# Kernel optimization log

Hardware: AMD Instinct MI355X
Metric: run time of the kernel (lower is better)

The kernel has to match this reference:

```python
import jax, jax.numpy as jnp
import numpy as np

H = 128; W = 128          # BEV grid (row_num_embed = col_num_embed = 128)
B = 1
CIN = 384; D = 256; NH = 8; NP = 4; NF = 128  # NF = num_feats of pos encoding
NLAYERS = 4               # 3 cross + 1 self


def setup_inputs() -> dict:
    key = jax.random.key(0)
    ks = jax.random.split(key, 32)
    s = 0.02
    rn = lambda k, shp: (jax.random.normal(k, shp, dtype=jnp.float32) * s)
    z = lambda shp: jnp.zeros(shp, jnp.float32)
    inp = {
        'query': jax.random.normal(ks[0], (B, CIN, H, W), jnp.float32),
        'value': jax.random.normal(ks[1], (B, CIN, H, W), jnp.float32),
        # 1x1 conv input projections (out, in)
        'conv_q_w': rn(ks[2], (D, CIN)), 'conv_q_b': z((D,)),
        'conv_v_w': rn(ks[3], (D, CIN)), 'conv_v_b': z((D,)),
        # learned positional embedding tables
        'row_embed': rn(ks[4], (H, NF)), 'col_embed': rn(ks[5], (W, NF)),
        # pre-attention linear layers (in, out)
        'lin_q_w': rn(ks[6], (D, D)), 'lin_q_b': z((D,)),
        'lin_v_w': rn(ks[7], (D, D)), 'lin_v_b': z((D,)),
        # stacked MSDeformAttn params for 4 layers
        'msda_off_w': rn(ks[8], (NLAYERS, D, NH * NP * 2)), 'msda_off_b': z((NLAYERS, NH * NP * 2)),
        'msda_aw_w': rn(ks[9], (NLAYERS, D, NH * NP)), 'msda_aw_b': z((NLAYERS, NH * NP)),
        'msda_vp_w': rn(ks[10], (NLAYERS, D, D)), 'msda_vp_b': z((NLAYERS, D)),
        'msda_op_w': rn(ks[11], (NLAYERS, D, D)), 'msda_op_b': z((NLAYERS, D)),
        # output MLP: 256 -> 128 -> 64 -> 384 with LayerNorm+ReLU between
        'out_w1': rn(ks[12], (D, D // 2)), 'out_b1': z((D // 2,)),
        'ln1_g': jnp.ones((D // 2,), jnp.float32), 'ln1_b': z((D // 2,)),
        'out_w2': rn(ks[13], (D // 2, D // 4)), 'out_b2': z((D // 4,)),
        'ln2_g': jnp.ones((D // 4,), jnp.float32), 'ln2_b': z((D // 4,)),
        'out_w3': rn(ks[14], (D // 4, CIN)), 'out_b3': z((CIN,)),
    }
    return inp


def _ln(x, g, b):
    mu = jnp.mean(x, -1, keepdims=True)
    var = jnp.mean(jnp.square(x - mu), -1, keepdims=True)
    return (x - mu) * jax.lax.rsqrt(var + 1e-5) * g + b


def reference(query, value, conv_q_w, conv_q_b, conv_v_w, conv_v_b, row_embed, col_embed,
              lin_q_w, lin_q_b, lin_v_w, lin_v_b,
              msda_off_w, msda_off_b, msda_aw_w, msda_aw_b,
              msda_vp_w, msda_vp_b, msda_op_w, msda_op_b,
              out_w1, out_b1, ln1_g, ln1_b, out_w2, out_b2, ln2_g, ln2_b, out_w3, out_b3):
    Bv, Cin, Hh, Ww = query.shape
    Nq = Hh * Ww
    HD = D // NH
    # 1x1 convs = per-pixel channel matmul; layout (Nq, B, D) = flatten(2).permute(2,0,1)
    q = jnp.einsum('bchw,dc->hwbd', query, conv_q_w).reshape(Nq, Bv, D) + conv_q_b
    v = jnp.einsum('bchw,dc->hwbd', value, conv_v_w).reshape(Nq, Bv, D) + conv_v_b
    # LearnedPositionalEncoding: cat([col_embed(x), row_embed(y)], -1)
    pos = jnp.concatenate([
        jnp.broadcast_to(col_embed[None, :Ww], (Hh, Ww, NF)),
        jnp.broadcast_to(row_embed[:Hh, None], (Hh, Ww, NF))], -1).reshape(Nq, 1, D)
    q = q @ lin_q_w + lin_q_b
    v = v @ lin_v_w + lin_v_b
    # reference points (pixel centers, normalized, (x, y) order)
    ry = (jnp.arange(Hh, dtype=q.dtype) + 0.5) / Hh
    rx = (jnp.arange(Ww, dtype=q.dtype) + 0.5) / Ww
    gx, gy = jnp.meshgrid(rx, ry, indexing='xy')  # (H, W)
    ref = jnp.stack([gx, gy], -1).reshape(1, Nq, 2)
    inv_wh = jnp.array([1.0 / Ww, 1.0 / Hh], dtype=q.dtype)

    def msda_layer(q_in, v_in, i):
        qp = q_in + pos                                   # query + query_pos
        val = (v_in @ msda_vp_w[i] + msda_vp_b[i]).transpose(1, 0, 2).reshape(Bv, Hh, Ww, NH, HD)
        off = (qp @ msda_off_w[i] + msda_off_b[i]).transpose(1, 0, 2).reshape(Bv, Nq, NH, NP, 2)
        aw = jax.nn.softmax((qp @ msda_aw_w[i] + msda_aw_b[i]).transpose(1, 0, 2)
                            .reshape(Bv, Nq, NH, NP), axis=-1)
        loc = ref[:, :, None, None, :] + off * inv_wh     # (B, Nq, NH, NP, 2) in [0,1]
        # bilinear sampling, zero padding, align_corners=False (grid_sample semantics)
        x = loc[..., 0] * Ww - 0.5
        y = loc[..., 1] * Hh - 0.5
        x0f = jnp.floor(x); y0f = jnp.floor(y)
        lx = (x - x0f).transpose(0, 2, 1, 3)              # (B, NH, Nq, NP)
        ly = (y - y0f).transpose(0, 2, 1, 3)
        x0 = x0f.astype(jnp.int32).transpose(0, 2, 1, 3)
        y0 = y0f.astype(jnp.int32).transpose(0, 2, 1, 3)
        vflat = val.transpose(0, 3, 1, 2, 4).reshape(Bv, NH, Hh * Ww, HD)
        awt = aw.transpose(0, 2, 1, 3)                    # (B, NH, Nq, NP)

        def corner(yi, xi, w):
            valid = (yi >= 0) & (yi < Hh) & (xi >= 0) & (xi < Ww)
            idx = (jnp.clip(yi, 0, Hh - 1) * Ww + jnp.clip(xi, 0, Ww - 1)).reshape(Bv, NH, Nq * NP, 1)
            g = jnp.take_along_axis(vflat, idx, axis=2).reshape(Bv, NH, Nq, NP, HD)
            return g * (w * valid.astype(w.dtype) * awt)[..., None]

        out = (corner(y0, x0, (1 - lx) * (1 - ly))
               + corner(y0, x0 + 1, lx * (1 - ly))
               + corner(y0 + 1, x0, (1 - lx) * ly)
               + corner(y0 + 1, x0 + 1, lx * ly)).sum(3)  # (B, NH, Nq, HD)
        out = out.transpose(2, 0, 1, 3).reshape(Nq, Bv, D)
        return out @ msda_op_w[i] + msda_op_b[i] + q_in   # residual (dropout=identity, eval)

    for i in range(3):                                    # cross layers: value features
        q = msda_layer(q, v, i)
    q = msda_layer(q, q, 3)                               # self layer: value = query

    h1 = jax.nn.relu(_ln(q @ out_w1 + out_b1, ln1_g, ln1_b))
    h2 = jax.nn.relu(_ln(h1 @ out_w2 + out_b2, ln2_g, ln2_b))
    out = h2 @ out_w3 + out_b3                            # (Nq, B, Cin)
    return out.transpose(1, 2, 0).reshape(Bv, Cin, Hh, Ww)
```

## Files before the change

kernel.cpp:

```cpp
#include <hip/hip_runtime.h>
#include <hip/hip_bf16.h>

#define NQ   16384
#define DIM  256

using bf16 = __hip_bfloat16;
using bf16x8 = __attribute__((ext_vector_type(8))) short;
using f32x4  = __attribute__((ext_vector_type(4))) float;

__device__ __forceinline__ float b2f(bf16 x) { return __bfloat162float(x); }
__device__ __forceinline__ bf16  f2b(float x) { return __float2bfloat16(x); }
__device__ __forceinline__ unsigned short f2bb(float x) {
    bf16 h = __float2bfloat16(x);
    return *(unsigned short*)&h;
}
__device__ __forceinline__ float us2f(unsigned short u) {
    unsigned int x = ((unsigned int)u) << 16;
    return __builtin_bit_cast(float, x);
}
__device__ __forceinline__ bf16x8 pack8(const float* f) {
    bf16x8 r;
#pragma unroll
    for (int j = 0; j < 8; ++j) r[j] = (short)f2bb(f[j]);
    return r;
}

__device__ __forceinline__ void xcd_map(int& sx, int& sy)
{
    const int gx  = gridDim.x;
    const int nwg = gridDim.x * gridDim.y;
    const int bid = blockIdx.y * gx + blockIdx.x;
    const int q = nwg >> 3, r = nwg & 7;
    const int xcd = bid & 7, sl = bid >> 3;
    const int s = (xcd < r ? xcd * (q + 1) : r * (q + 1) + (xcd - r) * q) + sl;
    sx = s % gx;
    sy = s / gx;
}

template<int MW, int NF, int KS>
__device__ __forceinline__ void gcore(
    bf16* __restrict__ Bs,
    const bf16* __restrict__ A, const bf16* __restrict__ Bgl,
    const float* __restrict__ bias, const bf16* __restrict__ res,
    const float* __restrict__ ce, const float* __restrict__ re,
    bf16* __restrict__ C, bf16* __restrict__ C2,
    int N, int n0, int m0)
{
    constexpr int K   = KS * 32;
    constexpr int LDB = K + 8;

    const int t    = threadIdx.x;
    const int lane = t & 63;
    const int wid  = t >> 6;
    const int lr   = lane & 15;
    const int lg   = lane >> 4;

    const bf16* Ab = A + (size_t)(m0 + wid * MW * 16 + lr) * K + lg * 8;

    bf16x8 af0[MW], af1[MW], af2[MW];
#pragma unroll
    for (int mi = 0; mi < MW; ++mi)
        af0[mi] = *(const bf16x8*)&Ab[(size_t)(mi * 16) * K + 0];
    if (KS > 1) {
#pragma unroll
        for (int mi = 0; mi < MW; ++mi)
            af1[mi] = *(const bf16x8*)&Ab[(size_t)(mi * 16) * K + 32];
    }

#pragma unroll
    for (int c = 0; c < NF * KS / 4; ++c) {
        const int id  = c * 256 + t;
        const int row = id / (KS * 4);
        const int kc  = id % (KS * 4);
        *(int4*)&Bs[row * LDB + kc * 8] = *(const int4*)&Bgl[(size_t)row * K + kc * 8];
    }
    __syncthreads();

    f32x4 acc[MW][NF];
#pragma unroll
    for (int i = 0; i < MW; ++i)
#pragma unroll
        for (int j = 0; j < NF; ++j) {
            f32x4 z = {0.f, 0.f, 0.f, 0.f};
            acc[i][j] = z;
        }

    bf16x8 bcur[NF], bnxt[NF];
#pragma unroll
    for (int jj = 0; jj < NF; ++jj)
        bcur[jj] = *(const bf16x8*)&Bs[(jj * 16 + lr) * LDB + lg * 8];

#pragma unroll
    for (int s = 0; s < KS; ++s) {
        if (s + 2 < KS) {
#pragma unroll
            for (int mi = 0; mi < MW; ++mi)
                af2[mi] = *(const bf16x8*)&Ab[(size_t)(mi * 16) * K + (s + 2) * 32];
        }
        if (s + 1 < KS) {
#pragma unroll
            for (int jj = 0; jj < NF; ++jj)
                bnxt[jj] = *(const bf16x8*)&Bs[(jj * 16 + lr) * LDB + (s + 1) * 32 + lg * 8];
        }
#pragma unroll
        for (int mi = 0; mi < MW; ++mi)
#pragma unroll
            for (int jj = 0; jj < NF; ++jj)
                acc[mi][jj] = __builtin_amdgcn_mfma_f32_16x16x32_bf16(
                    af0[mi], bcur[jj], acc[mi][jj], 0, 0, 0);
#pragma unroll
        for (int mi = 0; mi < MW; ++mi) { af0[mi] = af1[mi]; af1[mi] = af2[mi]; }
#pragma unroll
        for (int jj = 0; jj < NF; ++jj) bcur[jj] = bnxt[jj];
    }

    const bool dores = res != nullptr;
    const bool doqp  = C2 != nullptr;
#pragma unroll
    for (int mi = 0; mi < MW; ++mi) {
#pragma unroll
        for (int jj = 0; jj < NF; ++jj) {
            const int row0 = m0 + wid * MW * 16 + mi * 16 + lg * 4;
            const int col  = n0 + jj * 16 + lr;
            const float bvl = bias[col];
#pragma unroll
            for (int r = 0; r < 4; ++r) {
                const size_t off = (size_t)(row0 + r) * N + col;
                float v = acc[mi][jj][r] + bvl;
                if (dores) v += b2f(res[off]);
                C[off] = f2b(v);
                if (doqp) {
                    const int row = row0 + r;
                    const float pv = (col < 128)
                        ? ce[(row & 127) * 128 + col]
                        : re[(row >> 7) * 128 + (col - 128)];
                    C2[(size_t)row * 256 + col] = f2b(v + pv);
                }
            }
        }
    }
}

__device__ __forceinline__ void gcore_qv(
    bf16* __restrict__ Bs,
    const float* __restrict__ A, const bf16* __restrict__ Bgl,
    const float* __restrict__ bias,
    const float* __restrict__ ce, const float* __restrict__ re,
    bf16* __restrict__ C, bf16* __restrict__ C2,
    int n0, int m0)
{
    constexpr int K = 384, LDB = 192 + 8;

    const int t    = threadIdx.x;
    const int lane = t & 63;
    const int wid  = t >> 6;
    const int lr   = lane & 15;
    const int lg   = lane >> 4;

    const int rowb = m0 + wid * 16 + lr;

    float fa[5][8];
    auto loadA = [&](float f[8], int s) {
        const int k0 = s * 32 + lg * 8;
#pragma unroll
        for (int j = 0; j < 8; ++j)
            f[j] = A[(size_t)(k0 + j) * NQ + rowb];
    };
    auto stageB = [&](int h) {
#pragma unroll
        for (int c = 0; c < 6; ++c) {
            const int id  = c * 256 + t;
            const int row = id / 24;
            const int kc  = id % 24;
            *(int4*)&Bs[row * LDB + kc * 8] =
                *(const int4*)&Bgl[(size_t)row * K + h * 192 + kc * 8];
        }
    };

    loadA(fa[0], 0);
    loadA(fa[1], 1);
    loadA(fa[2], 2);
    loadA(fa[3], 3);
    stageB(0);
    __syncthreads();

    f32x4 acc[4];
#pragma unroll
    for (int j = 0; j < 4; ++j) { f32x4 z = {0.f, 0.f, 0.f, 0.f}; acc[j] = z; }

    bf16x8 bcur[4], bnxt[4];
#pragma unroll
    for (int jj = 0; jj < 4; ++jj)
        bcur[jj] = *(const bf16x8*)&Bs[(jj * 16 + lr) * LDB + lg * 8];

#pragma unroll
    for (int s = 0; s < 12; ++s) {
        const int sh = s % 6;
        if (s + 4 < 12) loadA(fa[(s + 4) % 5], s + 4);
        if (sh < 5) {
#pragma unroll
            for (int jj = 0; jj < 4; ++jj)
                bnxt[jj] = *(const bf16x8*)&Bs[(jj * 16 + lr) * LDB + (sh + 1) * 32 + lg * 8];
        }
        {
            const bf16x8 af = pack8(fa[s % 5]);
#pragma unroll
            for (int jj = 0; jj < 4; ++jj)
                acc[jj] = __builtin_amdgcn_mfma_f32_16x16x32_bf16(
                    af, bcur[jj], acc[jj], 0, 0, 0);
        }
        if (sh == 5 && s < 11) {
            __syncthreads();
            stageB(1);
            __syncthreads();
#pragma unroll
            for (int jj = 0; jj < 4; ++jj)
                bcur[jj] = *(const bf16x8*)&Bs[(jj * 16 + lr) * LDB + lg * 8];
        } else {
#pragma unroll
            for (int jj = 0; jj < 4; ++jj) bcur[jj] = bnxt[jj];
        }
    }

    const bool doqp = C2 != nullptr;
#pragma unroll
    for (int jj = 0; jj < 4; ++jj) {
        const int row0 = m0 + wid * 16 + lg * 4;
        const int col  = n0 + jj * 16 + lr;
        const float bvl = bias[col];
#pragma unroll
        for (int r = 0; r < 4; ++r) {
            const size_t off = (size_t)(row0 + r) * 256 + col;
            float v = acc[jj][r] + bvl;
            C[off] = f2b(v);
            if (doqp) {
                const int row = row0 + r;
                const float pv = (col < 128)
                    ? ce[(row & 127) * 128 + col]
                    : re[(row >> 7) * 128 + (col - 128)];
                C2[off] = f2b(v + pv);
            }
        }
    }
}

template<int MW, int KS>
__global__ __launch_bounds__(256)
void gmm_std(const bf16* __restrict__ A, const bf16* __restrict__ B,
             const float* __restrict__ bias, const bf16* __restrict__ res,
             const float* __restrict__ ce, const float* __restrict__ re,
             bf16* __restrict__ C, bf16* __restrict__ C2, int N)
{
    __shared__ bf16 Bs[64 * (KS * 32 + 8)];
    int sx, sy;
    xcd_map(sx, sy);
    const int n0 = sx * 64;
    gcore<MW, 4, KS>(Bs, A, B + (size_t)n0 * (KS * 32), bias, res, ce, re, C, C2,
                     N, n0, sy * (MW * 64));
}

__global__ __launch_bounds__(256)
void gmm_qv(const float* __restrict__ Qf, const bf16* __restrict__ WQ,
            const float* __restrict__ BQ, bf16* __restrict__ QA, bf16* __restrict__ QPb,
            const float* __restrict__ Vf, const bf16* __restrict__ WV,
            const float* __restrict__ BV, bf16* __restrict__ V,
            const float* __restrict__ ce, const float* __restrict__ re)
{
    __shared__ bf16 Bs[64 * (192 + 8)];
    int sx, sy;
    xcd_map(sx, sy);
    const int m0 = sy * 64;
    if (sx < 4) {
        const int n0 = sx * 64;
        gcore_qv(Bs, Qf, WQ + (size_t)n0 * 384, BQ, ce, re, QA, QPb, n0, m0);
    } else {
        const int n0 = (sx - 4) * 64;
        gcore_qv(Bs, Vf, WV + (size_t)n0 * 384, BV, nullptr, nullptr, V, nullptr, n0, m0);
    }
}

__global__ __launch_bounds__(256)
void gmm_vpall(const bf16* __restrict__ V, const bf16* __restrict__ WVP,
               const float* __restrict__ vp_b, bf16* __restrict__ VP,
               const bf16* __restrict__ QPb, const bf16* __restrict__ Boa,
               const float* __restrict__ boa, bf16* __restrict__ OA)
{
    __shared__ bf16 Bs[64 * (256 + 8)];
    int sx, sy;
    xcd_map(sx, sy);
    const int m0 = sy * 64;
    if (sx < 12) {
        const int layer = sx >> 2;
        const int nloc  = (sx & 3) * 64;
        gcore<1, 4, 8>(Bs, V, WVP + (size_t)sx * 64 * 256,
                       vp_b + layer * 256, nullptr, nullptr, nullptr,
                       VP + (size_t)layer * NQ * 256, nullptr, 256, nloc, m0);
    } else {
        const int n0 = (sx - 12) * 64;
        gcore<1, 4, 8>(Bs, QPb, Boa + (size_t)n0 * 256, boa, nullptr, nullptr, nullptr,
                       OA, nullptr, 128, n0, m0);
    }
}

__global__ __launch_bounds__(256)
void gmm_vo3(const bf16* __restrict__ cur, const bf16* __restrict__ Bvp,
             const float* __restrict__ bvp, bf16* __restrict__ T2,
             const bf16* __restrict__ QPb, const bf16* __restrict__ Boa,
             const float* __restrict__ boa, bf16* __restrict__ OA)
{
    __shared__ bf16 Bs[64 * (256 + 8)];
    int sx, sy;
    xcd_map(sx, sy);
    const int m0 = sy * 64;
    if (sx < 4) {
        const int n0 = sx * 64;
        gcore<1, 4, 8>(Bs, cur, Bvp + (size_t)n0 * 256, bvp, nullptr, nullptr, nullptr,
                       T2, nullptr, 256, n0, m0);
    } else {
        const int n0 = (sx - 4) * 64;
        gcore<1, 4, 8>(Bs, QPb, Boa + (size_t)n0 * 256, boa, nullptr, nullptr, nullptr,
                       OA, nullptr, 128, n0, m0);
    }
}

__global__ __launch_bounds__(256)
void gmm_out(const bf16* __restrict__ A, const bf16* __restrict__ B,
             const float* __restrict__ bias, float* __restrict__ out)
{
    constexpr int KS = 2, K = 64, LDB = K + 8;
    __shared__ bf16 Bs[64 * LDB];
    int sx, sy;
    xcd_map(sx, sy);
    const int n0 = sx * 64;
    const int m0 = sy * 64;

    const int t    = threadIdx.x;
    const int lane = t & 63;
    const int wid  = t >> 6;
    const int lr   = lane & 15;
    const int lg   = lane >> 4;

    const bf16* Ab = A + (size_t)(m0 + wid * 16 + lr) * K + lg * 8;
    const bf16* Bb = B + (size_t)n0 * K;

    bf16x8 af0 = *(const bf16x8*)&Ab[0];
    bf16x8 af1 = *(const bf16x8*)&Ab[32];

#pragma unroll
    for (int c = 0; c < 2; ++c) {
        const int id  = c * 256 + t;
        const int row = id >> 3, kc = id & 7;
        *(int4*)&Bs[row * LDB + kc * 8] = *(const int4*)&Bb[(size_t)row * K + kc * 8];
    }
    __syncthreads();

    f32x4 acc[4];
#pragma unroll
    for (int j = 0; j < 4; ++j) { f32x4 z = {0.f, 0.f, 0.f, 0.f}; acc[j] = z; }

#pragma unroll
    for (int s = 0; s < KS; ++s) {
        const bf16x8 af = s == 0 ? af0 : af1;
#pragma unroll
        for (int jj = 0; jj < 4; ++jj) {
            const bf16x8 bf = *(const bf16x8*)&Bs[(jj * 16 + lr) * LDB + s * 32 + lg * 8];
            acc[jj] = __builtin_amdgcn_mfma_f32_16x16x32_bf16(af, bf, acc[jj], 0, 0, 0);
        }
    }

    const int row0 = m0 + wid * 16 + lg * 4;
#pragma unroll
    for (int jj = 0; jj < 4; ++jj) {
        const int col = n0 + jj * 16 + lr;
        const float bvl = bias[col];
        float4 o;
        o.x = acc[jj][0] + bvl;
        o.y = acc[jj][1] + bvl;
        o.z = acc[jj][2] + bvl;
        o.w = acc[jj][3] + bvl;
        *(float4*)&out[(size_t)col * NQ + row0] = o;
    }
}

template<int NF, int KS>
__device__ __forceinline__ void gcore_ln(
    bf16* __restrict__ Bs,
    const bf16* __restrict__ A, const bf16* __restrict__ Bgl,
    const float* __restrict__ bias, bf16* __restrict__ C,
    const float* __restrict__ lng, const float* __restrict__ lnb,
    int N, int m0)
{
    constexpr int K    = KS * 32;
    constexpr int LDB  = K + 8;
    constexpr int NPAN = NF * 16;

    const int t    = threadIdx.x;
    const int lane = t & 63;
    const int wid  = t >> 6;
    const int lr   = lane & 15;
    const int lg   = lane >> 4;

#pragma unroll
    for (int c = 0; c < NF * KS / 4; ++c) {
        const int id  = c * 256 + t;
        const int row = id / (KS * 4);
        const int kc  = id % (KS * 4);
        *(int4*)&Bs[row * LDB + kc * 8] = *(const int4*)&Bgl[(size_t)row * K + kc * 8];
    }
    __syncthreads();

    f32x4 acc[NF];
#pragma unroll
    for (int j = 0; j < NF; ++j) { f32x4 z = {0.f, 0.f, 0.f, 0.f}; acc[j] = z; }

    const bf16* Ab = A + (size_t)(m0 + wid * 16 + lr) * K + lg * 8;

#pragma unroll
    for (int s = 0; s < KS; ++s) {
        bf16x8 af = *(const bf16x8*)&Ab[s * 32];
#pragma unroll
        for (int jj = 0; jj < NF; ++jj) {
            const bf16x8 bf = *(const bf16x8*)&Bs[(jj * 16 + lr) * LDB + s * 32 + lg * 8];
            acc[jj] = __builtin_amdgcn_mfma_f32_16x16x32_bf16(af, bf, acc[jj], 0, 0, 0);
        }
    }

    float bvl[NF], gv[NF], bb[NF];
#pragma unroll
    for (int jj = 0; jj < NF; ++jj) {
        const int col = jj * 16 + lr;
        bvl[jj] = bias[col]; gv[jj] = lng[col]; bb[jj] = lnb[col];
    }
#pragma unroll
    for (int r = 0; r < 4; ++r) {
        float v[NF];
        float s = 0.f;
#pragma unroll
        for (int jj = 0; jj < NF; ++jj) { v[jj] = acc[jj][r] + bvl[jj]; s += v[jj]; }
        s += __shfl_xor(s, 1); s += __shfl_xor(s, 2);
        s += __shfl_xor(s, 4); s += __shfl_xor(s, 8);
        const float mu = s * (1.f / NPAN);
        float vs = 0.f;
#pragma unroll
        for (int jj = 0; jj < NF; ++jj) { const float d = v[jj] - mu; vs += d * d; }
        vs += __shfl_xor(vs, 1); vs += __shfl_xor(vs, 2);
        vs += __shfl_xor(vs, 4); vs += __shfl_xor(vs, 8);
        const float rstd = rsqrtf(vs * (1.f / NPAN) + 1e-5f);
        const int row = m0 + wid * 16 + lg * 4 + r;
#pragma unroll
        for (int jj = 0; jj < NF; ++jj) {
            const float o = (v[jj] - mu) * rstd * gv[jj] + bb[jj];
            C[(size_t)row * N + jj * 16 + lr] = f2b(fmaxf(o, 0.f));
        }
    }
}

__global__ __launch_bounds__(256)
void gmm_mlp1(const bf16* __restrict__ A, const bf16* __restrict__ B,
              const float* __restrict__ bias, bf16* __restrict__ C,
              const float* __restrict__ g, const float* __restrict__ b)
{
    __shared__ bf16 Bs[128 * (256 + 8)];
    gcore_ln<8, 8>(Bs, A, B, bias, C, g, b, 128, blockIdx.y * 64);
}

__global__ __launch_bounds__(256)
void gmm_mlp2(const bf16* __restrict__ A, const bf16* __restrict__ B,
              const float* __restrict__ bias, bf16* __restrict__ C,
              const float* __restrict__ g, const float* __restrict__ b)
{
    __shared__ bf16 Bs[64 * (128 + 8)];
    gcore_ln<4, 4>(Bs, A, B, bias, C, g, b, 64, blockIdx.y * 64);
}

__global__ __launch_bounds__(256)
void prep_all(const float* __restrict__ vp_w, const float* __restrict__ op_w,
              const float* __restrict__ off_w, const float* __restrict__ aw_w,
              const float* __restrict__ off_b, const float* __restrict__ aw_b,
              const float* __restrict__ w1, const float* __restrict__ w2,
              const float* __restrict__ w3,
              bf16* __restrict__ WVP, bf16* __restrict__ WOP, bf16* __restrict__ WOA,
              bf16* __restrict__ WM1, bf16* __restrict__ WM2, bf16* __restrict__ WM3,
              float* __restrict__ OAB,
              const float* __restrict__ cqw, const float* __restrict__ cqb,
              const float* __restrict__ cvw, const float* __restrict__ cvb,
              const float* __restrict__ lqw, const float* __restrict__ lqb,
              const float* __restrict__ lvw, const float* __restrict__ lvb,
              bf16* __restrict__ WQc, bf16* __restrict__ WVc,
              float* __restrict__ BQc, float* __restrict__ BVc)
{
    __shared__ float tile[64][65];
    const int b = blockIdx.x;
    const int t = threadIdx.x;
    const int tr  = t >> 4;
    const int tc4 = (t & 15) * 4;

    if (b < 176) {
        const int ti = b;
        const float* src; bf16* dst; int K, N, k0, n0, Nt;
        if (ti < 64)       { const int l = ti >> 4, r = ti & 15; src = vp_w + l * 65536; dst = WVP + l * 65536; K = 256; N = 256; k0 = (r >> 2) * 64; n0 = (r & 3) * 64; Nt = 64; }
        else if (ti < 128) { const int l = (ti - 64) >> 4, r = (ti - 64) & 15; src = op_w + l * 65536; dst = WOP + l * 65536; K = 256; N = 256; k0 = (r >> 2) * 64; n0 = (r & 3) * 64; Nt = 64; }
        else if (ti < 144) { const int l = (ti - 128) >> 2, r = (ti - 128) & 3; src = off_w + l * 16384; dst = WOA + l * 32768; K = 256; N = 64; k0 = r * 64; n0 = 0; Nt = 64; }
        else if (ti < 160) { const int l = (ti - 144) >> 2, r = (ti - 144) & 3; src = aw_w + l * 8192; dst = WOA + l * 32768 + 16384; K = 256; N = 32; k0 = r * 64; n0 = 0; Nt = 32; }
        else if (ti < 168) { const int r = ti - 160; src = w1; dst = WM1; K = 256; N = 128; k0 = (r >> 1) * 64; n0 = (r & 1) * 64; Nt = 64; }
        else if (ti < 170) { const int r = ti - 168; src = w2; dst = WM2; K = 128; N = 64; k0 = r * 64; n0 = 0; Nt = 64; }
        else               { const int r = ti - 170; src = w3; dst = WM3; K = 64; N = 384; k0 = 0; n0 = r * 64; Nt = 64; }
#pragma unroll
        for (int i = 0; i < 4; ++i) {
            const int k = i * 16 + tr;
            if (tc4 < Nt) {
                const float4 vv = *(const float4*)&src[(size_t)(k0 + k) * N + n0 + tc4];
                tile[k][tc4 + 0] = vv.x; tile[k][tc4 + 1] = vv.y;
                tile[k][tc4 + 2] = vv.z; tile[k][tc4 + 3] = vv.w;
            }
        }
        __syncthreads();
#pragma unroll
        for (int i = 0; i < 4; ++i) {
            const int n = i * 16 + tr;
            if (n < Nt) {
                ushort4 o;
                o.x = f2bb(tile[tc4 + 0][n]); o.y = f2bb(tile[tc4 + 1][n]);
                o.z = f2bb(tile[tc4 + 2][n]); o.w = f2bb(tile[tc4 + 3][n]);
                *(ushort4*)&dst[(size_t)(n0 + n) * K + k0 + tc4] = o;
            }
        }
        return;
    }
    if (b < 192) {
        const int z0 = (b - 176) * 2048 + t * 8;
        const int l = z0 >> 13, r = z0 & 8191;
        bf16x8 zz = {0, 0, 0, 0, 0, 0, 0, 0};
        *(bf16x8*)&WOA[(size_t)l * 32768 + 24576 + r] = zz;
        return;
    }
    if (b < 961) {
        const int bb = b - 192;
        if (bb < 768) {
            const bool isq = bb < 384;
            const float* cw = isq ? cqw : cvw;
            const float* lw = isq ? lqw : lvw;
            bf16* W = isq ? WQc : WVc;
            const int idx = (bb % 384) * 256 + t;
            const int n = idx / 384, c = idx % 384;
            float s = 0.f;
            for (int d = 0; d < 256; ++d)
                s = fmaf(cw[d * 384 + c], lw[d * 256 + n], s);
            W[idx] = f2b(s);
        } else {
            const int n = t;
            float sq = lqb[n], sv = lvb[n];
            for (int d = 0; d < 256; ++d) {
                sq = fmaf(cqb[d], lqw[d * 256 + n], sq);
                sv = fmaf(cvb[d], lvw[d * 256 + n], sv);
            }
            BQc[n] = sq; BVc[n] = sv;
        }
        return;
    }
    {
        const int idx = (b - 961) * 256 + t;
        if (idx < 512) {
            const int l = idx >> 7, r = idx & 127;
            OAB[idx] = (r < 64) ? off_b[l * 64 + r] : (r < 96 ? aw_b[l * 32 + r - 64] : 0.f);
        }
    }
}

__global__ __launch_bounds__(256)
void sample_kernel(const bf16* __restrict__ val, const bf16* __restrict__ oa,
                   bf16* __restrict__ out)
{
    const int tid = threadIdx.x;
    const int pix = blockIdx.x * 8 + (tid >> 5);
    const int thr = tid & 31;
    const int head = thr >> 2;
    const int c0 = thr * 8;
    const float fx = (float)(pix & 127);
    const float fy = (float)(pix >> 7);
    const unsigned short* oap = (const unsigned short*)(oa + (size_t)pix * 128);
    const bf16x8 offs = *(const bf16x8*)&oap[head * 8];
    const ushort4 lg4 = *(const ushort4*)&oap[64 + head * 4];
    const float l0 = us2f(lg4.x), l1 = us2f(lg4.y), l2 = us2f(lg4.z), l3 = us2f(lg4.w);
    const float mx = fmaxf(fmaxf(l0, l1), fmaxf(l2, l3));
    const float e0 = __expf(l0 - mx), e1 = __expf(l1 - mx);
    const float e2 = __expf(l2 - mx), e3 = __expf(l3 - mx);
    const float inv = 1.f / (e0 + e1 + e2 + e3);
    const float aw4[4] = {e0 * inv, e1 * inv, e2 * inv, e3 * inv};

    float acc[8];
#pragma unroll
    for (int c = 0; c < 8; ++c) acc[c] = 0.f;

#pragma unroll
    for (int p = 0; p < 4; ++p) {
        const float x = fx + us2f((unsigned short)offs[p * 2 + 0]);
        const float y = fy + us2f((unsigned short)offs[p * 2 + 1]);
        const float x0f = floorf(x), y0f = floorf(y);
        const float lx = x - x0f, ly = y - y0f;
        const int x0 = (int)x0f, y0 = (int)y0f;
        const float a = aw4[p];
        const float wc[4] = {(1.f - lx) * (1.f - ly) * a, lx * (1.f - ly) * a,
                             (1.f - lx) * ly * a,         lx * ly * a};
        const int xs[4] = {x0, x0 + 1, x0, x0 + 1};
        const int ys[4] = {y0, y0, y0 + 1, y0 + 1};
#pragma unroll
        for (int k = 0; k < 4; ++k) {
            if ((unsigned)ys[k] < 128u && (unsigned)xs[k] < 128u) {
                const bf16x8 v = *(const bf16x8*)&val[(size_t)((ys[k] << 7) + xs[k]) * 256 + c0];
                const float w = wc[k];
#pragma unroll
                for (int c = 0; c < 8; ++c)
                    acc[c] = fmaf(us2f((unsigned short)v[c]), w, acc[c]);
            }
        }
    }
    bf16x8 o;
#pragma unroll
    for (int c = 0; c < 8; ++c) o[c] = (short)f2bb(acc[c]);
    *(bf16x8*)&out[(size_t)pix * 256 + c0] = o;
}

extern "C" void kernel_launch(void* const* d_in, const int* in_sizes, int n_in,
                              void* d_out, int out_size, void* d_ws, size_t ws_size,
                              hipStream_t stream)
{
    const float* query     = (const float*)d_in[0];
    const float* value     = (const float*)d_in[1];
    const float* conv_q_w  = (const float*)d_in[2];
    const float* conv_q_b  = (const float*)d_in[3];
    const float* conv_v_w  = (const float*)d_in[4];
    const float* conv_v_b  = (const float*)d_in[5];
    const float* row_embed = (const float*)d_in[6];
    const float* col_embed = (const float*)d_in[7];
    const float* lin_q_w   = (const float*)d_in[8];
    const float* lin_q_b   = (const float*)d_in[9];
    const float* lin_v_w   = (const float*)d_in[10];
    const float* lin_v_b   = (const float*)d_in[11];
    const float* off_w     = (const float*)d_in[12];
    const float* off_b     = (const float*)d_in[13];
    const float* aw_w      = (const float*)d_in[14];
    const float* aw_b      = (const float*)d_in[15];
    const float* vp_w      = (const float*)d_in[16];
    const float* vp_b      = (const float*)d_in[17];
    const float* op_w      = (const float*)d_in[18];
    const float* op_b      = (const float*)d_in[19];
    const float* out_w1    = (const float*)d_in[20];
    const float* out_b1    = (const float*)d_in[21];
    const float* ln1_g     = (const float*)d_in[22];
    const float* ln1_b     = (const float*)d_in[23];
    const float* out_w2    = (const float*)d_in[24];
    const float* out_b2    = (const float*)d_in[25];
    const float* ln2_g     = (const float*)d_in[26];
    const float* ln2_b     = (const float*)d_in[27];
    const float* out_w3    = (const float*)d_in[28];
    const float* out_b3    = (const float*)d_in[29];

    bf16* w = (bf16*)d_ws;
    auto alloc = [&](size_t n) { bf16* p = w; w += n; return p; };
    bf16* QA  = alloc((size_t)NQ * 256);
    bf16* QB  = alloc((size_t)NQ * 256);
    bf16* QPb = alloc((size_t)NQ * 256);
    bf16* V   = alloc((size_t)NQ * 256);
    bf16* T1  = alloc((size_t)NQ * 256);
    bf16* T2  = alloc((size_t)NQ * 256);
    bf16* VP  = alloc((size_t)3 * NQ * 256);
    bf16* OA  = alloc((size_t)NQ * 128);
    bf16* WQc = alloc(256 * 384);
    bf16* WVc = alloc(256 * 384);
    bf16* WVP = alloc(4 * 256 * 256);
    bf16* WOP = alloc(4 * 256 * 256);
    bf16* WOA = alloc(4 * 128 * 256);
    bf16* WM1 = alloc(128 * 256);
    bf16* WM2 = alloc(64 * 128);
    bf16* WM3 = alloc(384 * 64);
    float* fp = (float*)w;
    float* BQc = fp; fp += 256;
    float* BVc = fp; fp += 256;
    float* OAB = fp; fp += 512;

    const dim3 blk(256);

    prep_all<<<963, blk, 0, stream>>>(
        vp_w, op_w, off_w, aw_w, off_b, aw_b, out_w1, out_w2, out_w3,
        WVP, WOP, WOA, WM1, WM2, WM3, OAB,
        conv_q_w, conv_q_b, conv_v_w, conv_v_b,
        lin_q_w, lin_q_b, lin_v_w, lin_v_b,
        WQc, WVc, BQc, BVc);

    gmm_qv<<<dim3(8, 256), blk, 0, stream>>>(
        query, WQc, BQc, QA, QPb, value, WVc, BVc, V, col_embed, row_embed);
    gmm_vpall<<<dim3(14, 256), blk, 0, stream>>>(
        V, WVP, vp_b, VP, QPb, WOA, OAB, OA);

    bf16* cur = QA;
    bf16* nxt = QB;
    for (int i = 0; i < 4; ++i) {
        const bf16* valbuf;
        if (i < 3) {
            valbuf = VP + (size_t)i * NQ * 256;
            if (i > 0)
                gmm_std<1, 8><<<dim3(2, 256), blk, 0, stream>>>(
                    QPb, WOA + (size_t)i * 32768, OAB + i * 128, nullptr,
                    nullptr, nullptr, OA, nullptr, 128);
        } else {
            valbuf = T2;
            gmm_vo3<<<dim3(6, 256), blk, 0, stream>>>(
                cur, WVP + (size_t)3 * 65536, vp_b + 3 * 256, T2,
                QPb, WOA + (size_t)3 * 32768, OAB + 3 * 128, OA);
        }
        sample_kernel<<<2048, blk, 0, stream>>>(valbuf, OA, T1);
        gmm_std<1, 8><<<dim3(4, 256), blk, 0, stream>>>(
            T1, WOP + (size_t)i * 65536, op_b + i * 256, cur,
            col_embed, row_embed, nxt, QPb, 256);
        bf16* tmp = cur; cur = nxt; nxt = tmp;
    }

    gmm_mlp1<<<dim3(1, 256), blk, 0, stream>>>(cur, WM1, out_b1, T1, ln1_g, ln1_b);
    gmm_mlp2<<<dim3(1, 256), blk, 0, stream>>>(T1, WM2, out_b2, T2, ln2_g, ln2_b);
    gmm_out<<<dim3(6, 256), blk, 0, stream>>>(T2, WM3, out_b3, (float*)d_out);
}
```

Before: 218.0 us.

## Fuse offset/attention-weight projection GEMM into deformable sampling kernel

Computes the per-pixel offset and attention-logit projection (QPb times WOA) with MFMA inside the sampling kernel and keeps it in shared memory, so the separate OA GEMM launches and the OA global buffer go away. The V-projection and OA-projection combined kernels are split back into plain GEMMs. Sampling blocks grow to 512 threads covering 16 pixels. Each block now reloads the WOA weights from global memory, and the small GEMM adds latency ahead of the gather work.

```diff
diff --git a/kernel.cpp b/kernel.cpp
--- a/kernel.cpp
+++ b/kernel.cpp
@@ -281,46 +281,17 @@
 
 __global__ __launch_bounds__(256)
 void gmm_vpall(const bf16* __restrict__ V, const bf16* __restrict__ WVP,
-               const float* __restrict__ vp_b, bf16* __restrict__ VP,
-               const bf16* __restrict__ QPb, const bf16* __restrict__ Boa,
-               const float* __restrict__ boa, bf16* __restrict__ OA)
+               const float* __restrict__ vp_b, bf16* __restrict__ VP)
 {
     __shared__ bf16 Bs[64 * (256 + 8)];
     int sx, sy;
     xcd_map(sx, sy);
     const int m0 = sy * 64;
-    if (sx < 12) {
-        const int layer = sx >> 2;
-        const int nloc  = (sx & 3) * 64;
-        gcore<1, 4, 8>(Bs, V, WVP + (size_t)sx * 64 * 256,
-                       vp_b + layer * 256, nullptr, nullptr, nullptr,
-                       VP + (size_t)layer * NQ * 256, nullptr, 256, nloc, m0);
-    } else {
-        const int n0 = (sx - 12) * 64;
-        gcore<1, 4, 8>(Bs, QPb, Boa + (size_t)n0 * 256, boa, nullptr, nullptr, nullptr,
-                       OA, nullptr, 128, n0, m0);
-    }
-}
-
-__global__ __launch_bounds__(256)
-void gmm_vo3(const bf16* __restrict__ cur, const bf16* __restrict__ Bvp,
-             const float* __restrict__ bvp, bf16* __restrict__ T2,
-             const bf16* __restrict__ QPb, const bf16* __restrict__ Boa,
-             const float* __restrict__ boa, bf16* __restrict__ OA)
-{
-    __shared__ bf16 Bs[64 * (256 + 8)];
-    int sx, sy;
-    xcd_map(sx, sy);
-    const int m0 = sy * 64;
-    if (sx < 4) {
-        const int n0 = sx * 64;
-        gcore<1, 4, 8>(Bs, cur, Bvp + (size_t)n0 * 256, bvp, nullptr, nullptr, nullptr,
-                       T2, nullptr, 256, n0, m0);
-    } else {
-        const int n0 = (sx - 4) * 64;
-        gcore<1, 4, 8>(Bs, QPb, Boa + (size_t)n0 * 256, boa, nullptr, nullptr, nullptr,
-                       OA, nullptr, 128, n0, m0);
-    }
+    const int layer = sx >> 2;
+    const int nloc  = (sx & 3) * 64;
+    gcore<1, 4, 8>(Bs, V, WVP + (size_t)sx * 64 * 256,
+                   vp_b + layer * 256, nullptr, nullptr, nullptr,
+                   VP + (size_t)layer * NQ * 256, nullptr, 256, nloc, m0);
 }
 
 __global__ __launch_bounds__(256)
@@ -567,18 +538,45 @@
     }
 }
 
-__global__ __launch_bounds__(256)
-void sample_kernel(const bf16* __restrict__ val, const bf16* __restrict__ oa,
-                   bf16* __restrict__ out)
-{
+__global__ __launch_bounds__(512)
+void sample_fused(const bf16* __restrict__ val, const bf16* __restrict__ QPb,
+                  const bf16* __restrict__ Boa, const float* __restrict__ boa,
+                  bf16* __restrict__ out)
+{
+    __shared__ bf16 oa_s[16][136];
     const int tid = threadIdx.x;
-    const int pix = blockIdx.x * 8 + (tid >> 5);
-    const int thr = tid & 31;
+    const int p0 = blockIdx.x * 16;
+
+    {
+        const int lane = tid & 63;
+        const int w    = tid >> 6;
+        const int lr   = lane & 15;
+        const int lg   = lane >> 4;
+        const bf16* Ab = QPb + (size_t)(p0 + lr) * 256 + lg * 8;
+        const bf16* Bb = Boa + (size_t)(w * 16 + lr) * 256 + lg * 8;
+        f32x4 acc = {0.f, 0.f, 0.f, 0.f};
+#pragma unroll
+        for (int s = 0; s < 8; ++s) {
+            const bf16x8 af = *(const bf16x8*)&Ab[s * 32];
+            const bf16x8 bf = *(const bf16x8*)&Bb[s * 32];
+            acc = __builtin_amdgcn_mfma_f32_16x16x32_bf16(af, bf, acc, 0, 0, 0);
+        }
+        const int col = w * 16 + lr;
+        const float bvl = boa[col];
+#pragma unroll
+        for (int r = 0; r < 4; ++r)
+            oa_s[lg * 4 + r][col] = f2b(acc[r] + bvl);
+    }
+    __syncthreads();
+
+    const int pixl = tid >> 5;
+    const int thr  = tid & 31;
+    const int pix  = p0 + pixl;
     const int head = thr >> 2;
-    const int c0 = thr * 8;
+    const int c0   = thr * 8;
     const float fx = (float)(pix & 127);
     const float fy = (float)(pix >> 7);
-    const unsigned short* oap = (const unsigned short*)(oa + (size_t)pix * 128);
+    const unsigned short* oap = (const unsigned short*)&oa_s[pixl][0];
     const bf16x8 offs = *(const bf16x8*)&oap[head * 8];
     const ushort4 lg4 = *(const ushort4*)&oap[64 + head * 4];
     const float l0 = us2f(lg4.x), l1 = us2f(lg4.y), l2 = us2f(lg4.z), l3 = us2f(lg4.w);
@@ -665,7 +663,6 @@
     bf16* T1  = alloc((size_t)NQ * 256);
     bf16* T2  = alloc((size_t)NQ * 256);
     bf16* VP  = alloc((size_t)3 * NQ * 256);
-    bf16* OA  = alloc((size_t)NQ * 128);
     bf16* WQc = alloc(256 * 384);
     bf16* WVc = alloc(256 * 384);
     bf16* WVP = alloc(4 * 256 * 256);
@@ -690,8 +687,7 @@
 
     gmm_qv<<<dim3(8, 256), blk, 0, stream>>>(
         query, WQc, BQc, QA, QPb, value, WVc, BVc, V, col_embed, row_embed);
-    gmm_vpall<<<dim3(14, 256), blk, 0, stream>>>(
-        V, WVP, vp_b, VP, QPb, WOA, OAB, OA);
+    gmm_vpall<<<dim3(12, 256), blk, 0, stream>>>(V, WVP, vp_b, VP);
 
     bf16* cur = QA;
     bf16* nxt = QB;
@@ -699,17 +695,14 @@
         const bf16* valbuf;
         if (i < 3) {
             valbuf = VP + (size_t)i * NQ * 256;
-            if (i > 0)
-                gmm_std<1, 8><<<dim3(2, 256), blk, 0, stream>>>(
-                    QPb, WOA + (size_t)i * 32768, OAB + i * 128, nullptr,
-                    nullptr, nullptr, OA, nullptr, 128);
         } else {
+            gmm_std<1, 8><<<dim3(4, 256), blk, 0, stream>>>(
+                cur, WVP + (size_t)3 * 65536, vp_b + 3 * 256, nullptr,
+                nullptr, nullptr, T2, nullptr, 256);
             valbuf = T2;
-            gmm_vo3<<<dim3(6, 256), blk, 0, stream>>>(
-                cur, WVP + (size_t)3 * 65536, vp_b + 3 * 256, T2,
-                QPb, WOA + (size_t)3 * 32768, OAB + 3 * 128, OA);
-        }
-        sample_kernel<<<2048, blk, 0, stream>>>(valbuf, OA, T1);
+        }
+        sample_fused<<<1024, dim3(512), 0, stream>>>(
+            valbuf, QPb, WOA + (size_t)i * 32768, OAB + i * 128, T1);
         gmm_std<1, 8><<<dim3(4, 256), blk, 0, stream>>>(
             T1, WOP + (size_t)i * 65536, op_b + i * 256, cur,
             col_embed, row_embed, nxt, QPb, 256);
```

Result: slower. 257.4 us (+18.1%).

## Fuse output MLP three GEMMs with LayerNorms into single kernel

Applied to the files above, without the earlier changes.

Replaces the three output-MLP kernels (two GEMM+LayerNorm+ReLU and the final projection) with one kernel per 64-row tile that keeps the intermediate activations in shared memory. This removes two launches and the global round-trips of the hidden activations. In exchange the final projection runs with 256 blocks instead of 1536, and the larger shared-memory footprint limits occupancy during the output writes.

```diff
diff --git a/kernel.cpp b/kernel.cpp
--- a/kernel.cpp
+++ b/kernel.cpp
@@ -324,153 +324,160 @@
 }
 
 __global__ __launch_bounds__(256)
-void gmm_out(const bf16* __restrict__ A, const bf16* __restrict__ B,
-             const float* __restrict__ bias, float* __restrict__ out)
-{
-    constexpr int KS = 2, K = 64, LDB = K + 8;
-    __shared__ bf16 Bs[64 * LDB];
-    int sx, sy;
-    xcd_map(sx, sy);
-    const int n0 = sx * 64;
-    const int m0 = sy * 64;
+void mlp_tail(const bf16* __restrict__ A,
+              const bf16* __restrict__ WM1, const float* __restrict__ b1,
+              const float* __restrict__ g1, const float* __restrict__ lb1,
+              const bf16* __restrict__ WM2, const float* __restrict__ b2,
+              const float* __restrict__ g2, const float* __restrict__ lb2,
+              const bf16* __restrict__ WM3, const float* __restrict__ b3,
+              float* __restrict__ out)
+{
+    __shared__ bf16 Bs[128 * 264];
+    __shared__ bf16 h1[64][136];
+    __shared__ bf16 h2[64][72];
 
     const int t    = threadIdx.x;
     const int lane = t & 63;
     const int wid  = t >> 6;
     const int lr   = lane & 15;
     const int lg   = lane >> 4;
-
-    const bf16* Ab = A + (size_t)(m0 + wid * 16 + lr) * K + lg * 8;
-    const bf16* Bb = B + (size_t)n0 * K;
-
-    bf16x8 af0 = *(const bf16x8*)&Ab[0];
-    bf16x8 af1 = *(const bf16x8*)&Ab[32];
-
-#pragma unroll
-    for (int c = 0; c < 2; ++c) {
-        const int id  = c * 256 + t;
-        const int row = id >> 3, kc = id & 7;
-        *(int4*)&Bs[row * LDB + kc * 8] = *(const int4*)&Bb[(size_t)row * K + kc * 8];
+    const int m0   = blockIdx.x * 64;
+
+    {
+#pragma unroll
+        for (int c = 0; c < 16; ++c) {
+            const int id = c * 256 + t, row = id >> 5, kc = id & 31;
+            *(int4*)&Bs[row * 264 + kc * 8] = *(const int4*)&WM1[(size_t)row * 256 + kc * 8];
+        }
+        __syncthreads();
+        f32x4 acc[8];
+#pragma unroll
+        for (int j = 0; j < 8; ++j) { f32x4 z = {0.f, 0.f, 0.f, 0.f}; acc[j] = z; }
+        const bf16* Ab = A + (size_t)(m0 + wid * 16 + lr) * 256 + lg * 8;
+#pragma unroll
+        for (int s = 0; s < 8; ++s) {
+            const bf16x8 af = *(const bf16x8*)&Ab[s * 32];
+#pragma unroll
+            for (int jj = 0; jj < 8; ++jj) {
+                const bf16x8 bf = *(const bf16x8*)&Bs[(jj * 16 + lr) * 264 + s * 32 + lg * 8];
+                acc[jj] = __builtin_amdgcn_mfma_f32_16x16x32_bf16(af, bf, acc[jj], 0, 0, 0);
+            }
+        }
+        float bvl[8], gv[8], bb[8];
+#pragma unroll
+        for (int jj = 0; jj < 8; ++jj) {
+            const int col = jj * 16 + lr;
+            bvl[jj] = b1[col]; gv[jj] = g1[col]; bb[jj] = lb1[col];
+        }
+#pragma unroll
+        for (int r = 0; r < 4; ++r) {
+            float v[8];
+            float s = 0.f;
+#pragma unroll
+            for (int jj = 0; jj < 8; ++jj) { v[jj] = acc[jj][r] + bvl[jj]; s += v[jj]; }
+            s += __shfl_xor(s, 1); s += __shfl_xor(s, 2);
+            s += __shfl_xor(s, 4); s += __shfl_xor(s, 8);
+            const float mu = s * (1.f / 128.f);
+            float vs = 0.f;
+#pragma unroll
+            for (int jj = 0; jj < 8; ++jj) { const float d = v[jj] - mu; vs += d * d; }
+            vs += __shfl_xor(vs, 1); vs += __shfl_xor(vs, 2);
+            vs += __shfl_xor(vs, 4); vs += __shfl_xor(vs, 8);
+            const float rstd = rsqrtf(vs * (1.f / 128.f) + 1e-5f);
+            const int row = wid * 16 + lg * 4 + r;
+#pragma unroll
+            for (int jj = 0; jj < 8; ++jj) {
+                const float o = (v[jj] - mu) * rstd * gv[jj] + bb[jj];
+                h1[row][jj * 16 + lr] = f2b(fmaxf(o, 0.f));
+            }
+        }
     }
     __syncthreads();
 
-    f32x4 acc[4];
-#pragma unroll
-    for (int j = 0; j < 4; ++j) { f32x4 z = {0.f, 0.f, 0.f, 0.f}; acc[j] = z; }
-
-#pragma unroll
-    for (int s = 0; s < KS; ++s) {
-        const bf16x8 af = s == 0 ? af0 : af1;
+    {
+#pragma unroll
+        for (int c = 0; c < 4; ++c) {
+            const int id = c * 256 + t, row = id >> 4, kc = id & 15;
+            *(int4*)&Bs[row * 136 + kc * 8] = *(const int4*)&WM2[(size_t)row * 128 + kc * 8];
+        }
+        __syncthreads();
+        f32x4 acc[4];
+#pragma unroll
+        for (int j = 0; j < 4; ++j) { f32x4 z = {0.f, 0.f, 0.f, 0.f}; acc[j] = z; }
+#pragma unroll
+        for (int s = 0; s < 4; ++s) {
+            const bf16x8 af = *(const bf16x8*)&h1[wid * 16 + lr][s * 32 + lg * 8];
+#pragma unroll
+            for (int jj = 0; jj < 4; ++jj) {
+                const bf16x8 bf = *(const bf16x8*)&Bs[(jj * 16 + lr) * 136 + s * 32 + lg * 8];
+                acc[jj] = __builtin_amdgcn_mfma_f32_16x16x32_bf16(af, bf, acc[jj], 0, 0, 0);
+            }
+        }
+        float bvl[4], gv[4], bb[4];
 #pragma unroll
         for (int jj = 0; jj < 4; ++jj) {
-            const bf16x8 bf = *(const bf16x8*)&Bs[(jj * 16 + lr) * LDB + s * 32 + lg * 8];
-            acc[jj] = __builtin_amdgcn_mfma_f32_16x16x32_bf16(af, bf, acc[jj], 0, 0, 0);
-        }
-    }
-
-    const int row0 = m0 + wid * 16 + lg * 4;
-#pragma unroll
-    for (int jj = 0; jj < 4; ++jj) {
-        const int col = n0 + jj * 16 + lr;
-        const float bvl = bias[col];
-        float4 o;
-        o.x = acc[jj][0] + bvl;
-        o.y = acc[jj][1] + bvl;
-        o.z = acc[jj][2] + bvl;
-        o.w = acc[jj][3] + bvl;
-        *(float4*)&out[(size_t)col * NQ + row0] = o;
-    }
-}
-
-template<int NF, int KS>
-__device__ __forceinline__ void gcore_ln(
-    bf16* __restrict__ Bs,
-    const bf16* __restrict__ A, const bf16* __restrict__ Bgl,
-    const float* __restrict__ bias, bf16* __restrict__ C,
-    const float* __restrict__ lng, const float* __restrict__ lnb,
-    int N, int m0)
-{
-    constexpr int K    = KS * 32;
-    constexpr int LDB  = K + 8;
-    constexpr int NPAN = NF * 16;
-
-    const int t    = threadIdx.x;
-    const int lane = t & 63;
-    const int wid  = t >> 6;
-    const int lr   = lane & 15;
-    const int lg   = lane >> 4;
-
-#pragma unroll
-    for (int c = 0; c < NF * KS / 4; ++c) {
-        const int id  = c * 256 + t;
-        const int row = id / (KS * 4);
-        const int kc  = id % (KS * 4);
-        *(int4*)&Bs[row * LDB + kc * 8] = *(const int4*)&Bgl[(size_t)row * K + kc * 8];
+            const int col = jj * 16 + lr;
+            bvl[jj] = b2[col]; gv[jj] = g2[col]; bb[jj] = lb2[col];
+        }
+#pragma unroll
+        for (int r = 0; r < 4; ++r) {
+            float v[4];
+            float s = 0.f;
+#pragma unroll
+            for (int jj = 0; jj < 4; ++jj) { v[jj] = acc[jj][r] + bvl[jj]; s += v[jj]; }
+            s += __shfl_xor(s, 1); s += __shfl_xor(s, 2);
+            s += __shfl_xor(s, 4); s += __shfl_xor(s, 8);
+            const float mu = s * (1.f / 64.f);
+            float vs = 0.f;
+#pragma unroll
+            for (int jj = 0; jj < 4; ++jj) { const float d = v[jj] - mu; vs += d * d; }
+            vs += __shfl_xor(vs, 1); vs += __shfl_xor(vs, 2);
+            vs += __shfl_xor(vs, 4); vs += __shfl_xor(vs, 8);
+            const float rstd = rsqrtf(vs * (1.f / 64.f) + 1e-5f);
+            const int row = wid * 16 + lg * 4 + r;
+#pragma unroll
+            for (int jj = 0; jj < 4; ++jj) {
+                const float o = (v[jj] - mu) * rstd * gv[jj] + bb[jj];
+                h2[row][jj * 16 + lr] = f2b(fmaxf(o, 0.f));
+            }
+        }
     }
     __syncthreads();
 
-    f32x4 acc[NF];
-#pragma unroll
-    for (int j = 0; j < NF; ++j) { f32x4 z = {0.f, 0.f, 0.f, 0.f}; acc[j] = z; }
-
-    const bf16* Ab = A + (size_t)(m0 + wid * 16 + lr) * K + lg * 8;
-
-#pragma unroll
-    for (int s = 0; s < KS; ++s) {
-        bf16x8 af = *(const bf16x8*)&Ab[s * 32];
-#pragma unroll
-        for (int jj = 0; jj < NF; ++jj) {
-            const bf16x8 bf = *(const bf16x8*)&Bs[(jj * 16 + lr) * LDB + s * 32 + lg * 8];
-            acc[jj] = __builtin_amdgcn_mfma_f32_16x16x32_bf16(af, bf, acc[jj], 0, 0, 0);
-        }
-    }
-
-    float bvl[NF], gv[NF], bb[NF];
-#pragma unroll
-    for (int jj = 0; jj < NF; ++jj) {
-        const int col = jj * 16 + lr;
-        bvl[jj] = bias[col]; gv[jj] = lng[col]; bb[jj] = lnb[col];
-    }
-#pragma unroll
-    for (int r = 0; r < 4; ++r) {
-        float v[NF];
-        float s = 0.f;
-#pragma unroll
-        for (int jj = 0; jj < NF; ++jj) { v[jj] = acc[jj][r] + bvl[jj]; s += v[jj]; }
-        s += __shfl_xor(s, 1); s += __shfl_xor(s, 2);
-        s += __shfl_xor(s, 4); s += __shfl_xor(s, 8);
-        const float mu = s * (1.f / NPAN);
-        float vs = 0.f;
-#pragma unroll
-        for (int jj = 0; jj < NF; ++jj) { const float d = v[jj] - mu; vs += d * d; }
-        vs += __shfl_xor(vs, 1); vs += __shfl_xor(vs, 2);
-        vs += __shfl_xor(vs, 4); vs += __shfl_xor(vs, 8);
-        const float rstd = rsqrtf(vs * (1.f / NPAN) + 1e-5f);
-        const int row = m0 + wid * 16 + lg * 4 + r;
-#pragma unroll
-        for (int jj = 0; jj < NF; ++jj) {
-            const float o = (v[jj] - mu) * rstd * gv[jj] + bb[jj];
-            C[(size_t)row * N + jj * 16 + lr] = f2b(fmaxf(o, 0.f));
-        }
-    }
-}
-
-__global__ __launch_bounds__(256)
-void gmm_mlp1(const bf16* __restrict__ A, const bf16* __restrict__ B,
-              const float* __restrict__ bias, bf16* __restrict__ C,
-              const float* __restrict__ g, const float* __restrict__ b)
-{
-    __shared__ bf16 Bs[128 * (256 + 8)];
-    gcore_ln<8, 8>(Bs, A, B, bias, C, g, b, 128, blockIdx.y * 64);
-}
-
-__global__ __launch_bounds__(256)
-void gmm_mlp2(const bf16* __restrict__ A, const bf16* __restrict__ B,
-              const float* __restrict__ bias, bf16* __restrict__ C,
-              const float* __restrict__ g, const float* __restrict__ b)
-{
-    __shared__ bf16 Bs[64 * (128 + 8)];
-    gcore_ln<4, 4>(Bs, A, B, bias, C, g, b, 64, blockIdx.y * 64);
+    {
+#pragma unroll
+        for (int c = 0; c < 12; ++c) {
+            const int id = c * 256 + t, row = id >> 3, kc = id & 7;
+            *(int4*)&Bs[row * 72 + kc * 8] = *(const int4*)&WM3[(size_t)row * 64 + kc * 8];
+        }
+        __syncthreads();
+        const bf16x8 af0 = *(const bf16x8*)&h2[wid * 16 + lr][lg * 8];
+        const bf16x8 af1 = *(const bf16x8*)&h2[wid * 16 + lr][32 + lg * 8];
+        f32x4 acc[24];
+#pragma unroll
+        for (int j = 0; j < 24; ++j) { f32x4 z = {0.f, 0.f, 0.f, 0.f}; acc[j] = z; }
+#pragma unroll
+        for (int s = 0; s < 2; ++s) {
+            const bf16x8 af = s == 0 ? af0 : af1;
+#pragma unroll
+            for (int jj = 0; jj < 24; ++jj) {
+                const bf16x8 bf = *(const bf16x8*)&Bs[(jj * 16 + lr) * 72 + s * 32 + lg * 8];
+                acc[jj] = __builtin_amdgcn_mfma_f32_16x16x32_bf16(af, bf, acc[jj], 0, 0, 0);
+            }
+        }
+        const int row0 = m0 + wid * 16 + lg * 4;
+#pragma unroll
+        for (int jj = 0; jj < 24; ++jj) {
+            const int col = jj * 16 + lr;
+            const float bvl = b3[col];
+            float4 o;
+            o.x = acc[jj][0] + bvl;
+            o.y = acc[jj][1] + bvl;
+            o.z = acc[jj][2] + bvl;
+            o.w = acc[jj][3] + bvl;
+            *(float4*)&out[(size_t)col * NQ + row0] = o;
+        }
+    }
 }
 
 __global__ __launch_bounds__(256)
@@ -716,7 +723,8 @@
         bf16* tmp = cur; cur = nxt; nxt = tmp;
     }
 
-    gmm_mlp1<<<dim3(1, 256), blk, 0, stream>>>(cur, WM1, out_b1, T1, ln1_g, ln1_b);
-    gmm_mlp2<<<dim3(1, 256), blk, 0, stream>>>(T1, WM2, out_b2, T2, ln2_g, ln2_b);
-    gmm_out<<<dim3(6, 256), blk, 0, stream>>>(T2, WM3, out_b3, (float*)d_out);
-}
+    mlp_tail<<<256, blk, 0, stream>>>(
+        cur, WM1, out_b1, ln1_g, ln1_b,
+        WM2, out_b2, ln2_g, ln2_b,
+        WM3, out_b3, (float*)d_out);
+}
```

Result: faster. 211.5 us (median of 2 runs) (-3.0%).
